# Optimization experiments

Hardware: AMD Instinct MI355X
Metric: run time of the kernel (lower is better)

The kernel has to match this reference:

```python
import jax, jax.numpy as jnp
import numpy as np

E = 1024          # embd_size
HS = 64           # head_size
NH = E // HS      # num heads = 16
B, T = 2, 2048


def setup_inputs() -> dict:
    key = jax.random.key(0)
    ks = jax.random.split(key, 9)
    s = 1.0 / np.sqrt(E)
    inp = {
        "embd_q": jax.random.normal(ks[0], (B, T, E), dtype=jnp.float32),
        # torch nn.Linear weights are [out, in]; y = x @ W.T + b
        "Wq": jax.random.uniform(ks[1], (E, E), jnp.float32, -s, s),
        "bq": jax.random.uniform(ks[2], (E,), jnp.float32, -s, s),
        "Wk": jax.random.uniform(ks[3], (E, E), jnp.float32, -s, s),
        "bk": jax.random.uniform(ks[4], (E,), jnp.float32, -s, s),
        "Wv": jax.random.uniform(ks[5], (E, E), jnp.float32, -s, s),
        "bv": jax.random.uniform(ks[6], (E,), jnp.float32, -s, s),
        "Wo": jax.random.uniform(ks[7], (E, E), jnp.float32, -s, s),
        "bo": jax.random.uniform(ks[8], (E,), jnp.float32, -s, s),
    }
    return inp


def reference(embd_q, Wq, bq, Wk, bk, Wv, bv, Wo, bo):
    b, t, e = embd_q.shape
    q = embd_q @ Wq.T + bq
    k = embd_q @ Wk.T + bk
    v = embd_q @ Wv.T + bv
    # [B, NH, T, HS]
    q = q.reshape(b, t, NH, HS).transpose(0, 2, 1, 3)
    k = k.reshape(b, t, NH, HS).transpose(0, 2, 1, 3)
    v = v.reshape(b, t, NH, HS).transpose(0, 2, 1, 3)
    w = jnp.einsum("bhqd,bhkd->bhqk", q, k) / jnp.sqrt(jnp.float32(HS))
    causal = jnp.triu(jnp.ones((t, t), dtype=bool), k=1)  # True above diag
    w = jnp.where(causal[None, None, :, :], -jnp.inf, w)
    w = jax.nn.softmax(w, axis=-1)
    a = jnp.einsum("bhqk,bhkd->bhqd", w, v)
    a = a.transpose(0, 2, 1, 3).reshape(b, t, e)
    return a @ Wo.T + bo
```

## Files before the change

kernel.cpp:

```cpp
#include <hip/hip_runtime.h>

typedef unsigned short u16;
typedef __bf16 bf16x8 __attribute__((ext_vector_type(8)));
typedef __bf16 bf16x4 __attribute__((ext_vector_type(4)));
typedef __bf16 bf16x2 __attribute__((ext_vector_type(2)));
typedef short s16x4 __attribute__((ext_vector_type(4)));
typedef float f32x4 __attribute__((ext_vector_type(4)));

#define Mdim 4096
#define Ndim 1024
#define Kdim 1024

__device__ __forceinline__ u16 f2bf(float f) {
    unsigned u = __float_as_uint(f);
    u += 0x7FFF + ((u >> 16) & 1);
    return (u16)(u >> 16);
}

__device__ __forceinline__ void gl_lds16(const u16* g, u16* l) {
    __builtin_amdgcn_global_load_lds(
        (const __attribute__((address_space(1))) unsigned int*)g,
        (__attribute__((address_space(3))) unsigned int*)l, 16, 0, 0);
}

__device__ __forceinline__ f32x4 mfma16(s16x4 a, s16x4 b, f32x4 c) {
#if __has_builtin(__builtin_amdgcn_mfma_f32_16x16x16_bf16)
    return __builtin_amdgcn_mfma_f32_16x16x16_bf16(
        __builtin_bit_cast(bf16x4, a), __builtin_bit_cast(bf16x4, b), c, 0, 0, 0);
#else
    return __builtin_amdgcn_mfma_f32_16x16x16bf16_1k(a, b, c, 0, 0, 0);
#endif
}

#if __has_builtin(__builtin_amdgcn_exp2f)
#define EXP2(x) __builtin_amdgcn_exp2f(x)
#else
#define EXP2(x) exp2f(x)
#endif

__device__ __forceinline__ s16x4 pack4bf(float a, float b, float c, float d) {
#if __has_builtin(__builtin_amdgcn_cvt_pk_bf16_f32)
    union { struct { bf16x2 lo, hi; } v; s16x4 s; } u;
    u.v.lo = __builtin_amdgcn_cvt_pk_bf16_f32(a, b);
    u.v.hi = __builtin_amdgcn_cvt_pk_bf16_f32(c, d);
    return u.s;
#else
    s16x4 r;
    r.x = (short)f2bf(a); r.y = (short)f2bf(b);
    r.z = (short)f2bf(c); r.w = (short)f2bf(d);
    return r;
#endif
}

__global__ __launch_bounds__(256) void cast_all(
    const float* __restrict__ X,
    const float* __restrict__ Wq, const float* __restrict__ Wk,
    const float* __restrict__ Wv, const float* __restrict__ Wo,
    u16* __restrict__ Xb,
    u16* __restrict__ Wqb, u16* __restrict__ Wkb,
    u16* __restrict__ Wvb, u16* __restrict__ Wob) {
    size_t i4 = (size_t)blockIdx.x * blockDim.x + threadIdx.x;
    size_t flat = i4 * 4;
    const float* src;
    u16* dst;
    size_t off;
    if (flat < (size_t)4194304) {
        src = X; dst = Xb; off = flat;
    } else {
        size_t r = flat - 4194304;
        int w = (int)(r >> 20);
        off = r & 1048575;
        src = (w == 0) ? Wq : (w == 1) ? Wk : (w == 2) ? Wv : Wo;
        dst = (w == 0) ? Wqb : (w == 1) ? Wkb : (w == 2) ? Wvb : Wob;
    }
    float4 v = *(const float4*)(src + off);
    ushort4 o;
    o.x = f2bf(v.x); o.y = f2bf(v.y); o.z = f2bf(v.z); o.w = f2bf(v.w);
    *(ushort4*)(dst + off) = o;
}

template <int BN>
__device__ __forceinline__ void gemm_core(const u16* __restrict__ A,
                                          const u16* __restrict__ Bw,
                                          const float* __restrict__ bias,
                                          void* __restrict__ out,
                                          int n0, int mode) {
    __shared__ __align__(16) u16 At[128 * 64];
    __shared__ __align__(16) u16 Bt[BN * 64];
    const int tid = threadIdx.x, w = tid >> 6, lane = tid & 63;
    const int quad = lane >> 4, l16 = lane & 15;
    const int wm = w & 1, wn = w >> 1;
    const int m0 = blockIdx.x * 128;
    constexpr int NTN = BN / 32;
    f32x4 acc[4][NTN] = {};
    const int r8 = lane >> 3, c8 = lane & 7;

    for (int k0 = 0; k0 < Kdim; k0 += 64) {
        __syncthreads();
#pragma unroll
        for (int i = 0; i < 4; ++i) {
            int row = w * 32 + i * 8 + r8;
            int j = c8 ^ (row & 7);
            gl_lds16(A + (size_t)(m0 + row) * Kdim + k0 + j * 8,
                     &At[(w * 32 + i * 8) * 64]);
        }
#pragma unroll
        for (int i = 0; i < BN / 32; ++i) {
            int row = w * (BN / 4) + i * 8 + r8;
            int j = c8 ^ (row & 7);
            gl_lds16(Bw + (size_t)(n0 + row) * Kdim + k0 + j * 8,
                     &Bt[(w * (BN / 4) + i * 8) * 64]);
        }
        __syncthreads();
#pragma unroll
        for (int ks = 0; ks < 2; ++ks) {
            bf16x8 af[4], bf[NTN];
#pragma unroll
            for (int mt = 0; mt < 4; ++mt) {
                int r = wm * 64 + mt * 16 + l16;
                af[mt] = *(const bf16x8*)&At[r * 64 + ((ks * 4 + quad) ^ (r & 7)) * 8];
            }
#pragma unroll
            for (int nt = 0; nt < NTN; ++nt) {
                int r = wn * (BN / 2) + nt * 16 + l16;
                bf[nt] = *(const bf16x8*)&Bt[r * 64 + ((ks * 4 + quad) ^ (r & 7)) * 8];
            }
#pragma unroll
            for (int mt = 0; mt < 4; ++mt)
#pragma unroll
                for (int nt = 0; nt < NTN; ++nt)
                    acc[mt][nt] = __builtin_amdgcn_mfma_f32_16x16x32_bf16(
                        af[mt], bf[nt], acc[mt][nt], 0, 0, 0);
        }
    }

#pragma unroll
    for (int nt = 0; nt < NTN; ++nt) {
        int n = n0 + wn * (BN / 2) + nt * 16 + l16;
        float bb = bias[n];
#pragma unroll
        for (int mt = 0; mt < 4; ++mt) {
            int mbase = m0 + wm * 64 + mt * 16 + quad * 4;
            if (mode == 2) {
                int b = mbase >> 11, t = mbase & 2047;
                int h = n >> 6, d = n & 63;
                ushort4 pk;
                pk.x = f2bf(acc[mt][nt][0] + bb);
                pk.y = f2bf(acc[mt][nt][1] + bb);
                pk.z = f2bf(acc[mt][nt][2] + bb);
                pk.w = f2bf(acc[mt][nt][3] + bb);
                *(ushort4*)&((u16*)out)[(((size_t)(b * 16 + h) * 64 + d) << 11) + t] = pk;
            } else if (mode == 0) {
#pragma unroll
                for (int r = 0; r < 4; ++r) {
                    int m = mbase + r;
                    int b = m >> 11, t = m & 2047, h = n >> 6, d = n & 63;
                    ((u16*)out)[(((size_t)(b * 16 + h) * 2048 + t) << 6) + d] =
                        f2bf(acc[mt][nt][r] + bb);
                }
            } else {
#pragma unroll
                for (int r = 0; r < 4; ++r)
                    ((float*)out)[(size_t)(mbase + r) * Ndim + n] = acc[mt][nt][r] + bb;
            }
        }
    }
}

__global__ __launch_bounds__(256, 2) void qkv_gemm(
    const u16* __restrict__ Xb,
    const u16* __restrict__ Wqb, const u16* __restrict__ Wkb, const u16* __restrict__ Wvb,
    const float* __restrict__ bq, const float* __restrict__ bk, const float* __restrict__ bv,
    u16* __restrict__ Qw, u16* __restrict__ Kw, u16* __restrict__ VTw) {
    const int y = blockIdx.y;
    const int z = y >> 3;
    const int n0 = (y & 7) * 128;
    const u16* Bw = (z == 0) ? Wqb : (z == 1) ? Wkb : Wvb;
    const float* bias = (z == 0) ? bq : (z == 1) ? bk : bv;
    void* out = (z == 0) ? (void*)Qw : (z == 1) ? (void*)Kw : (void*)VTw;
    gemm_core<128>(Xb, Bw, bias, out, n0, (z == 2) ? 2 : 0);
}

__global__ __launch_bounds__(256, 2) void out_gemm(
    const u16* __restrict__ Aatt, const u16* __restrict__ Wob,
    const float* __restrict__ bo, float* __restrict__ out) {
    gemm_core<64>(Aatt, Wob, bo, out, blockIdx.y * 64, 1);
}

__global__ __launch_bounds__(256, 2) void flash_attn(
    const u16* __restrict__ Q, const u16* __restrict__ K,
    const u16* __restrict__ VT, u16* __restrict__ Aatt) {
    __shared__ __align__(16) u16 KLds[4][2][2048];
    __shared__ __align__(16) u16 VLds[4][2][2048];

    const int tid = threadIdx.x, w = tid >> 6, lane = tid & 63;
    const int quad = lane >> 4, l16 = lane & 15;
    const int g = blockIdx.x;
    const int bh = g & 31;
    const int sg = g >> 5;
    const int Q0 = (15 - sg) * 128;
    const int qlo = Q0 + w * 32;
    const int ntw = (qlo >> 5) + 1;

    const u16* Qh  = Q  + (size_t)bh * 131072;
    const u16* Kh  = K  + (size_t)bh * 131072;
    const u16* VTh = VT + (size_t)bh * 131072;

    bf16x8 qf[2][2];
#pragma unroll
    for (int qt = 0; qt < 2; ++qt)
#pragma unroll
        for (int ks = 0; ks < 2; ++ks)
            qf[qt][ks] = *(const bf16x8*)(Qh + (size_t)(qlo + qt * 16 + l16) * 64
                                             + ks * 32 + quad * 8);

    f32x4 o[2][4] = {};
    float lsum[2] = {0.f, 0.f};

    const int kr = lane >> 3;
    const int kj = lane & 7;
    const int vr = lane >> 2;
    const int vj = lane & 3;

#define STAGE(buf_, kt_)                                                         \
    {                                                                            \
        const u16* kg_ = Kh + (size_t)((kt_) * 32) * 64;                         \
        _Pragma("unroll")                                                        \
        for (int i_ = 0; i_ < 4; ++i_) {                                         \
            int row_ = i_ * 8 + kr;                                              \
            gl_lds16(kg_ + (size_t)row_ * 64 + (kj ^ (row_ & 7)) * 8,            \
                     &KLds[w][buf_][i_ * 512]);                                  \
        }                                                                        \
        const u16* vg_ = VTh + (kt_) * 32;                                       \
        _Pragma("unroll")                                                        \
        for (int i_ = 0; i_ < 4; ++i_) {                                         \
            int d_ = i_ * 16 + vr;                                               \
            gl_lds16(vg_ + (size_t)d_ * 2048 + (vj ^ ((d_ >> 1) & 3)) * 8,       \
                     &VLds[w][buf_][i_ * 512]);                                  \
        }                                                                        \
    }

    STAGE(0, 0);
    const float c1 = 0.18033688011112042f;

    for (int kt = 0; kt < ntw; ++kt) {
        if (kt + 1 < ntw) {
            STAGE((kt + 1) & 1, kt + 1);
            asm volatile("s_waitcnt vmcnt(8)" ::: "memory");
        } else {
            asm volatile("s_waitcnt vmcnt(0)" ::: "memory");
        }
        const u16* kb  = &KLds[w][kt & 1][0];
        const u16* vbp = &VLds[w][kt & 1][0];
        const bool dm = (kt == ntw - 1);
#pragma unroll
        for (int c = 0; c < 2; ++c) {
            bf16x8 ka[2];
#pragma unroll
            for (int ks = 0; ks < 2; ++ks) {
                int r = c * 16 + l16;
                ka[ks] = *(const bf16x8*)&kb[r * 64 + (((ks << 2) + quad) ^ (l16 & 7)) * 8];
            }
            s16x4 vf[4];
#pragma unroll
            for (int dt = 0; dt < 4; ++dt) {
                int d = dt * 16 + l16;
                int phys = ((c << 1) + (quad >> 1)) ^ ((d >> 1) & 3);
                vf[dt] = *(const s16x4*)&vbp[d * 32 + phys * 8 + (quad & 1) * 4];
            }
#pragma unroll
            for (int qt = 0; qt < 2; ++qt) {
                f32x4 z = {};
                z = __builtin_amdgcn_mfma_f32_16x16x32_bf16(ka[0], qf[qt][0], z, 0, 0, 0);
                z = __builtin_amdgcn_mfma_f32_16x16x32_bf16(ka[1], qf[qt][1], z, 0, 0, 0);
                float p[4];
                if (dm) {
                    int q = qlo + qt * 16 + l16;
                    int kkb = kt * 32 + c * 16 + quad * 4;
#pragma unroll
                    for (int r = 0; r < 4; ++r)
                        p[r] = (kkb + r > q) ? 0.f : EXP2(z[r] * c1);
                } else {
#pragma unroll
                    for (int r = 0; r < 4; ++r) p[r] = EXP2(z[r] * c1);
                }
                lsum[qt] += (p[0] + p[1]) + (p[2] + p[3]);
                s16x4 pa = pack4bf(p[0], p[1], p[2], p[3]);
#pragma unroll
                for (int dt = 0; dt < 4; ++dt)
                    o[qt][dt] = mfma16(pa, vf[dt], o[qt][dt]);
            }
        }
    }

    const int b = bh >> 4, h = bh & 15;
#pragma unroll
    for (int qt = 0; qt < 2; ++qt) {
        float l = lsum[qt];
        l += __shfl_xor(l, 16);
        l += __shfl_xor(l, 32);
        float inv = 1.0f / l;
        float rinv[4];
#pragma unroll
        for (int r = 0; r < 4; ++r)
            rinv[r] = __shfl(inv, (lane & 48) + quad * 4 + r);
#pragma unroll
        for (int dt = 0; dt < 4; ++dt) {
            int e = h * 64 + dt * 16 + l16;
#pragma unroll
            for (int r = 0; r < 4; ++r) {
                int t = qlo + qt * 16 + quad * 4 + r;
                Aatt[((size_t)(b * 2048 + t)) * 1024 + e] = f2bf(o[qt][dt][r] * rinv[r]);
            }
        }
    }
}

extern "C" void kernel_launch(void* const* d_in, const int* in_sizes, int n_in,
                              void* d_out, int out_size, void* d_ws, size_t ws_size,
                              hipStream_t stream) {
    const float* X  = (const float*)d_in[0];
    const float* Wq = (const float*)d_in[1];
    const float* bq = (const float*)d_in[2];
    const float* Wk = (const float*)d_in[3];
    const float* bk = (const float*)d_in[4];
    const float* Wv = (const float*)d_in[5];
    const float* bv = (const float*)d_in[6];
    const float* Wo = (const float*)d_in[7];
    const float* bo = (const float*)d_in[8];

    char* ws = (char*)d_ws;
    const size_t MB = 1 << 20;
    u16* Xb   = (u16*)(ws);
    u16* Wqb  = (u16*)(ws + 8  * MB);
    u16* Wkb  = (u16*)(ws + 10 * MB);
    u16* Wvb  = (u16*)(ws + 12 * MB);
    u16* Wob  = (u16*)(ws + 14 * MB);
    u16* Qw   = (u16*)(ws + 16 * MB);
    u16* Kw   = (u16*)(ws + 24 * MB);
    u16* VTw  = (u16*)(ws + 32 * MB);
    u16* Aatt = (u16*)(ws + 40 * MB);

    cast_all<<<8192, 256, 0, stream>>>(X, Wq, Wk, Wv, Wo, Xb, Wqb, Wkb, Wvb, Wob);
    qkv_gemm<<<dim3(32, 24), 256, 0, stream>>>(Xb, Wqb, Wkb, Wvb, bq, bk, bv, Qw, Kw, VTw);
    flash_attn<<<dim3(512), 256, 0, stream>>>(Qw, Kw, VTw, Aatt);
    out_gemm<<<dim3(32, 16), 256, 0, stream>>>(Aatt, Wob, bo, (float*)d_out);
}
```

Before: 189.0 us.

## Split attention KV range across warps with LDS reduction instead of per-warp query blocks

Each block now handles a single 32-row query tile, and its four warps stride over key tiles in an interleaved pattern. Partial outputs and row sums are combined through shared memory at the end, and the results are written with vectorized stores. K/V staging through LDS is replaced by direct register loads with double buffering, and the grid grows fourfold with launch bounds raised to 3 blocks per SM. This targets causal load imbalance and low occupancy. The cost is a cross-warp reduction and uncoalesced direct global loads of the V-transpose fragments.

```diff
diff --git a/kernel.cpp b/kernel.cpp
--- a/kernel.cpp
+++ b/kernel.cpp
@@ -187,20 +187,19 @@
     gemm_core<64>(Aatt, Wob, bo, out, blockIdx.y * 64, 1);
 }
 
-__global__ __launch_bounds__(256, 2) void flash_attn(
+__global__ __launch_bounds__(256, 3) void flash_attn(
     const u16* __restrict__ Q, const u16* __restrict__ K,
     const u16* __restrict__ VT, u16* __restrict__ Aatt) {
-    __shared__ __align__(16) u16 KLds[4][2][2048];
-    __shared__ __align__(16) u16 VLds[4][2][2048];
+    __shared__ __align__(16) float oLds[4 * 2048];
+    __shared__ float lsumLds[4][32];
 
     const int tid = threadIdx.x, w = tid >> 6, lane = tid & 63;
     const int quad = lane >> 4, l16 = lane & 15;
     const int g = blockIdx.x;
     const int bh = g & 31;
-    const int sg = g >> 5;
-    const int Q0 = (15 - sg) * 128;
-    const int qlo = Q0 + w * 32;
-    const int ntw = (qlo >> 5) + 1;
+    const int j = 63 - (g >> 5);
+    const int qbase = j * 32;
+    const int ntw = j + 1;
 
     const u16* Qh  = Q  + (size_t)bh * 131072;
     const u16* Kh  = K  + (size_t)bh * 131072;
@@ -211,108 +210,116 @@
     for (int qt = 0; qt < 2; ++qt)
 #pragma unroll
         for (int ks = 0; ks < 2; ++ks)
-            qf[qt][ks] = *(const bf16x8*)(Qh + (size_t)(qlo + qt * 16 + l16) * 64
+            qf[qt][ks] = *(const bf16x8*)(Qh + (size_t)(qbase + qt * 16 + l16) * 64
                                              + ks * 32 + quad * 8);
 
     f32x4 o[2][4] = {};
     float lsum[2] = {0.f, 0.f};
-
-    const int kr = lane >> 3;
-    const int kj = lane & 7;
-    const int vr = lane >> 2;
-    const int vj = lane & 3;
-
-#define STAGE(buf_, kt_)                                                         \
-    {                                                                            \
-        const u16* kg_ = Kh + (size_t)((kt_) * 32) * 64;                         \
-        _Pragma("unroll")                                                        \
-        for (int i_ = 0; i_ < 4; ++i_) {                                         \
-            int row_ = i_ * 8 + kr;                                              \
-            gl_lds16(kg_ + (size_t)row_ * 64 + (kj ^ (row_ & 7)) * 8,            \
-                     &KLds[w][buf_][i_ * 512]);                                  \
-        }                                                                        \
-        const u16* vg_ = VTh + (kt_) * 32;                                       \
-        _Pragma("unroll")                                                        \
-        for (int i_ = 0; i_ < 4; ++i_) {                                         \
-            int d_ = i_ * 16 + vr;                                               \
-            gl_lds16(vg_ + (size_t)d_ * 2048 + (vj ^ ((d_ >> 1) & 3)) * 8,       \
-                     &VLds[w][buf_][i_ * 512]);                                  \
-        }                                                                        \
-    }
-
-    STAGE(0, 0);
     const float c1 = 0.18033688011112042f;
 
-    for (int kt = 0; kt < ntw; ++kt) {
-        if (kt + 1 < ntw) {
-            STAGE((kt + 1) & 1, kt + 1);
-            asm volatile("s_waitcnt vmcnt(8)" ::: "memory");
-        } else {
-            asm volatile("s_waitcnt vmcnt(0)" ::: "memory");
-        }
-        const u16* kb  = &KLds[w][kt & 1][0];
-        const u16* vbp = &VLds[w][kt & 1][0];
-        const bool dm = (kt == ntw - 1);
-#pragma unroll
-        for (int c = 0; c < 2; ++c) {
-            bf16x8 ka[2];
-#pragma unroll
-            for (int ks = 0; ks < 2; ++ks) {
-                int r = c * 16 + l16;
-                ka[ks] = *(const bf16x8*)&kb[r * 64 + (((ks << 2) + quad) ^ (l16 & 7)) * 8];
-            }
-            s16x4 vf[4];
-#pragma unroll
-            for (int dt = 0; dt < 4; ++dt) {
-                int d = dt * 16 + l16;
-                int phys = ((c << 1) + (quad >> 1)) ^ ((d >> 1) & 3);
-                vf[dt] = *(const s16x4*)&vbp[d * 32 + phys * 8 + (quad & 1) * 4];
-            }
-#pragma unroll
-            for (int qt = 0; qt < 2; ++qt) {
-                f32x4 z = {};
-                z = __builtin_amdgcn_mfma_f32_16x16x32_bf16(ka[0], qf[qt][0], z, 0, 0, 0);
-                z = __builtin_amdgcn_mfma_f32_16x16x32_bf16(ka[1], qf[qt][1], z, 0, 0, 0);
-                float p[4];
-                if (dm) {
-                    int q = qlo + qt * 16 + l16;
-                    int kkb = kt * 32 + c * 16 + quad * 4;
-#pragma unroll
-                    for (int r = 0; r < 4; ++r)
-                        p[r] = (kkb + r > q) ? 0.f : EXP2(z[r] * c1);
-                } else {
-#pragma unroll
-                    for (int r = 0; r < 4; ++r) p[r] = EXP2(z[r] * c1);
-                }
-                lsum[qt] += (p[0] + p[1]) + (p[2] + p[3]);
-                s16x4 pa = pack4bf(p[0], p[1], p[2], p[3]);
-#pragma unroll
-                for (int dt = 0; dt < 4; ++dt)
-                    o[qt][dt] = mfma16(pa, vf[dt], o[qt][dt]);
-            }
-        }
-    }
-
-    const int b = bh >> 4, h = bh & 15;
+#define LOAD_TILE(kt_, ka_, vf_)                                               \
+    {                                                                          \
+        const u16* kp_ = Kh + (size_t)(kt_) * 2048;                            \
+        const u16* vp_ = VTh + (kt_) * 32;                                     \
+        _Pragma("unroll")                                                      \
+        for (int c_ = 0; c_ < 2; ++c_) {                                       \
+            _Pragma("unroll")                                                  \
+            for (int ks_ = 0; ks_ < 2; ++ks_)                                  \
+                ka_[c_][ks_] = *(const bf16x8*)(kp_ + (c_ * 16 + l16) * 64     \
+                                                + ks_ * 32 + quad * 8);        \
+            _Pragma("unroll")                                                  \
+            for (int dt_ = 0; dt_ < 4; ++dt_)                                  \
+                vf_[c_][dt_] = *(const s16x4*)(vp_ + (size_t)(dt_ * 16 + l16) * 2048 \
+                                               + c_ * 16 + quad * 4);          \
+        }                                                                      \
+    }
+
+#define COMPUTE_TILE(kt_, ka_, vf_)                                            \
+    {                                                                          \
+        const bool dm_ = ((kt_) == ntw - 1);                                   \
+        _Pragma("unroll")                                                      \
+        for (int c_ = 0; c_ < 2; ++c_) {                                       \
+            _Pragma("unroll")                                                  \
+            for (int qt_ = 0; qt_ < 2; ++qt_) {                                \
+                f32x4 z_ = {};                                                 \
+                z_ = __builtin_amdgcn_mfma_f32_16x16x32_bf16(                  \
+                    ka_[c_][0], qf[qt_][0], z_, 0, 0, 0);                      \
+                z_ = __builtin_amdgcn_mfma_f32_16x16x32_bf16(                  \
+                    ka_[c_][1], qf[qt_][1], z_, 0, 0, 0);                      \
+                float p_[4];                                                   \
+                if (dm_) {                                                     \
+                    int q_ = qbase + qt_ * 16 + l16;                           \
+                    int kkb_ = (kt_) * 32 + c_ * 16 + quad * 4;                \
+                    _Pragma("unroll")                                          \
+                    for (int r_ = 0; r_ < 4; ++r_)                             \
+                        p_[r_] = (kkb_ + r_ > q_) ? 0.f : EXP2(z_[r_] * c1);   \
+                } else {                                                       \
+                    _Pragma("unroll")                                          \
+                    for (int r_ = 0; r_ < 4; ++r_) p_[r_] = EXP2(z_[r_] * c1); \
+                }                                                              \
+                lsum[qt_] += (p_[0] + p_[1]) + (p_[2] + p_[3]);                \
+                s16x4 pa_ = pack4bf(p_[0], p_[1], p_[2], p_[3]);               \
+                _Pragma("unroll")                                              \
+                for (int dt_ = 0; dt_ < 4; ++dt_)                              \
+                    o[qt_][dt_] = mfma16(pa_, vf_[c_][dt_], o[qt_][dt_]);      \
+            }                                                                  \
+        }                                                                      \
+    }
+
+    bf16x8 kaA[2][2], kaB[2][2];
+    s16x4 vfA[2][4], vfB[2][4];
+    int kt = w;
+    if (kt < ntw) {
+        LOAD_TILE(kt, kaA, vfA);
+        while (true) {
+            int nx = kt + 4;
+            if (nx < ntw) LOAD_TILE(nx, kaB, vfB);
+            COMPUTE_TILE(kt, kaA, vfA);
+            kt = nx;
+            if (kt >= ntw) break;
+            nx = kt + 4;
+            if (nx < ntw) LOAD_TILE(nx, kaA, vfA);
+            COMPUTE_TILE(kt, kaB, vfB);
+            kt = nx;
+            if (kt >= ntw) break;
+        }
+    }
+
 #pragma unroll
     for (int qt = 0; qt < 2; ++qt) {
         float l = lsum[qt];
         l += __shfl_xor(l, 16);
         l += __shfl_xor(l, 32);
+        if (lane < 16) lsumLds[w][qt * 16 + lane] = l;
+#pragma unroll
+        for (int dt = 0; dt < 4; ++dt)
+#pragma unroll
+            for (int r = 0; r < 4; ++r)
+                oLds[w * 2048 + (qt * 16 + quad * 4 + r) * 64 + dt * 16 + l16] =
+                    o[qt][dt][r];
+    }
+    __syncthreads();
+
+    {
+        const int q = tid >> 3, d = (tid & 7) * 8;
+        float l = lsumLds[0][q] + lsumLds[1][q] + lsumLds[2][q] + lsumLds[3][q];
         float inv = 1.0f / l;
-        float rinv[4];
-#pragma unroll
-        for (int r = 0; r < 4; ++r)
-            rinv[r] = __shfl(inv, (lane & 48) + quad * 4 + r);
-#pragma unroll
-        for (int dt = 0; dt < 4; ++dt) {
-            int e = h * 64 + dt * 16 + l16;
-#pragma unroll
-            for (int r = 0; r < 4; ++r) {
-                int t = qlo + qt * 16 + quad * 4 + r;
-                Aatt[((size_t)(b * 2048 + t)) * 1024 + e] = f2bf(o[qt][dt][r] * rinv[r]);
-            }
-        }
+        f32x4 a0 = {}, a1 = {};
+#pragma unroll
+        for (int ww = 0; ww < 4; ++ww) {
+            a0 += *(const f32x4*)&oLds[ww * 2048 + q * 64 + d];
+            a1 += *(const f32x4*)&oLds[ww * 2048 + q * 64 + d + 4];
+        }
+        const int b = bh >> 4, h = bh & 15;
+        const int t = qbase + q;
+        ushort4 p0, p1;
+        p0.x = f2bf(a0[0] * inv); p0.y = f2bf(a0[1] * inv);
+        p0.z = f2bf(a0[2] * inv); p0.w = f2bf(a0[3] * inv);
+        p1.x = f2bf(a1[0] * inv); p1.y = f2bf(a1[1] * inv);
+        p1.z = f2bf(a1[2] * inv); p1.w = f2bf(a1[3] * inv);
+        u16* dst = Aatt + ((size_t)(b * 2048 + t)) * 1024 + h * 64 + d;
+        *(ushort4*)dst = p0;
+        *(ushort4*)(dst + 4) = p1;
     }
 }
 
@@ -343,6 +350,6 @@
 
     cast_all<<<8192, 256, 0, stream>>>(X, Wq, Wk, Wv, Wo, Xb, Wqb, Wkb, Wvb, Wob);
     qkv_gemm<<<dim3(32, 24), 256, 0, stream>>>(Xb, Wqb, Wkb, Wvb, bq, bk, bv, Qw, Kw, VTw);
-    flash_attn<<<dim3(512), 256, 0, stream>>>(Qw, Kw, VTw, Aatt);
+    flash_attn<<<dim3(2048), 256, 0, stream>>>(Qw, Kw, VTw, Aatt);
     out_gemm<<<dim3(32, 16), 256, 0, stream>>>(Aatt, Wob, bo, (float*)d_out);
 }
```

Result: slower. 229.2 us (+21.3%).
